# Kernel tuning notes

Hardware: AMD Instinct MI355X
Metric: run time of the kernel (lower is better)

## Reference

```python
import jax, jax.numpy as jnp
import numpy as np

N_QUBITS = 4
N_LAYERS = 3
N_OUTPUTS = 4
BATCH = 1048576


def _ry(t):
    # RY(t) = [[cos(t/2), -sin(t/2)], [sin(t/2), cos(t/2)]]; t may be scalar or (B,)
    c = jnp.cos(t / 2)
    s = jnp.sin(t / 2)
    m = jnp.stack([jnp.stack([c, -s], -1), jnp.stack([s, c], -1)], -2)
    return m.astype(jnp.complex64)


def _rx(t):
    c = jnp.cos(t / 2).astype(jnp.complex64)
    s = jnp.sin(t / 2).astype(jnp.complex64)
    return jnp.stack([jnp.stack([c, -1j * s], -1), jnp.stack([-1j * s, c], -1)], -2)


def _rz(t):
    e = jnp.exp(-1j * t.astype(jnp.complex64) / 2)  # exp(-i t/2)
    z = jnp.zeros_like(e)
    return jnp.stack([jnp.stack([e, z], -1), jnp.stack([z, jnp.conj(e)], -1)], -2)


def _apply_1q(state, U, q):
    # shared 2x2 gate U on wire q; state: (B, 2,2,2,2)
    s = jnp.moveaxis(state, q + 1, -1)
    s = jnp.einsum('ij,...j->...i', U, s)
    return jnp.moveaxis(s, -1, q + 1)


def _apply_1q_batched(state, U, q):
    # per-sample 2x2 gate U: (B,2,2) on wire q
    s = jnp.moveaxis(state, q + 1, -1)  # (B, ..., 2)
    s = jnp.einsum('bij,b...j->b...i', U, s)
    return jnp.moveaxis(s, -1, q + 1)


def _apply_cnot(state, c, t):
    s = jnp.moveaxis(state, (c + 1, t + 1), (-2, -1))  # (..., ctrl, tgt)
    s = jnp.stack([s[..., 0, :], s[..., 1, ::-1]], axis=-2)
    return jnp.moveaxis(s, (-2, -1), (c + 1, t + 1))


def setup_inputs() -> dict:
    key = jax.random.key(0)
    kx, kw = jax.random.split(key)
    x = jax.random.normal(kx, (BATCH, 2), dtype=jnp.float32)
    weights = jax.random.normal(kw, (N_LAYERS, N_QUBITS, 3), dtype=jnp.float32) * 0.1
    return {"x": x, "weights": weights}


def reference(x, weights):
    B = x.shape[0]
    # |0...0> state, batched
    state = jnp.zeros((B,) + (2,) * N_QUBITS, jnp.complex64)
    state = state.at[(slice(None),) + (0,) * N_QUBITS].set(1.0)
    # data encoding: RY(inputs[i % 2]) on wire i (per-sample angles)
    for i in range(N_QUBITS):
        state = _apply_1q_batched(state, _ry(x[:, i % 2]), i)
    # variational layers (shared angles)
    for l in range(N_LAYERS):
        for i in range(N_QUBITS):
            state = _apply_1q(state, _rx(weights[l, i, 0]), i)
            state = _apply_1q(state, _ry(weights[l, i, 1]), i)
            state = _apply_1q(state, _rz(weights[l, i, 2]), i)
        for i in range(N_QUBITS):
            state = _apply_cnot(state, i, (i + 1) % N_QUBITS)
    probs = state.real ** 2 + state.imag ** 2  # (B,2,2,2,2)
    outs = []
    for q in range(N_OUTPUTS):
        p = jnp.moveaxis(probs, q + 1, 1).reshape(B, 2, -1).sum(-1)
        outs.append(p[:, 0] - p[:, 1])  # <Z_q>
    return jnp.stack(outs, -1)  # (B, N_OUTPUTS)
```

## Files before the change

### kernel.cpp

```cpp
#include <hip/hip_runtime.h>
#include <hip/hip_bf16.h>


__device__ __forceinline__ float2 mul2(float2 a, float2 b) {
    return make_float2(a.x * b.x, a.y * b.y);
}
__device__ __forceinline__ float2 fma2(float s, float2 a, float2 b) {
    return make_float2(fmaf(s, a.x, b.x), fmaf(s, a.y, b.y));
}
__device__ __forceinline__ float2 fma22(float2 s, float2 a, float2 b) {
    return make_float2(fmaf(s.x, a.x, b.x), fmaf(s.y, a.y, b.y));
}

__global__ __launch_bounds__(256) void qnn_fused(const float2* __restrict__ x,
                                                 const float* __restrict__ w,
                                                 float4* __restrict__ out,
                                                 int B) {
    __shared__ float Ur[16][16];
    __shared__ float Ui[16][16];
    __shared__ __align__(16) float Csh[100];
    const int t = threadIdx.x;

    if (t < 100) Csh[t] = 0.0f;

    if (t < 16) {
        float ar[16], ai[16];
#pragma unroll
        for (int i = 0; i < 16; i++) { ar[i] = (i == t) ? 1.0f : 0.0f; ai[i] = 0.0f; }

#pragma unroll
        for (int l = 0; l < 3; l++) {
#pragma unroll
            for (int wq = 0; wq < 4; wq++) {
                const int st = 1 << (3 - wq);
                float th, s, c;
                th = w[(l * 4 + wq) * 3 + 0] * 0.5f;
                __sincosf(th, &s, &c);
#pragma unroll
                for (int lo = 0; lo < 16; lo++) if (!(lo & st)) {
                    const int hi = lo | st;
                    const float arl = ar[lo], ail = ai[lo], arh = ar[hi], aih = ai[hi];
                    ar[lo] = c * arl + s * aih;
                    ai[lo] = c * ail - s * arh;
                    ar[hi] = c * arh + s * ail;
                    ai[hi] = c * aih - s * arl;
                }
                th = w[(l * 4 + wq) * 3 + 1] * 0.5f;
                __sincosf(th, &s, &c);
#pragma unroll
                for (int lo = 0; lo < 16; lo++) if (!(lo & st)) {
                    const int hi = lo | st;
                    const float arl = ar[lo], ail = ai[lo], arh = ar[hi], aih = ai[hi];
                    ar[lo] = c * arl - s * arh;
                    ai[lo] = c * ail - s * aih;
                    ar[hi] = s * arl + c * arh;
                    ai[hi] = s * ail + c * aih;
                }
                th = w[(l * 4 + wq) * 3 + 2] * 0.5f;
                __sincosf(th, &s, &c);
#pragma unroll
                for (int lo = 0; lo < 16; lo++) if (!(lo & st)) {
                    const int hi = lo | st;
                    const float arl = ar[lo], ail = ai[lo], arh = ar[hi], aih = ai[hi];
                    ar[lo] = c * arl + s * ail;
                    ai[lo] = c * ail - s * arl;
                    ar[hi] = c * arh - s * aih;
                    ai[hi] = c * aih + s * arh;
                }
            }
#pragma unroll
            for (int ci = 0; ci < 4; ci++) {
                const int cst = 1 << (3 - ci);
                const int tst = 1 << (3 - ((ci + 1) & 3));
#pragma unroll
                for (int k = 0; k < 16; k++) if ((k & cst) && !(k & tst)) {
                    const int k2 = k | tst;
                    const float tr = ar[k], ti = ai[k];
                    ar[k] = ar[k2]; ai[k] = ai[k2];
                    ar[k2] = tr;    ai[k2] = ti;
                }
            }
        }
#pragma unroll
        for (int i = 0; i < 16; i++) { Ur[i][t] = ar[i]; Ui[i][t] = ai[i]; }
    }
    __syncthreads();

    {
        const int i = t >> 4;
        const int j = t & 15;
        float m0 = 0.f, m1 = 0.f, m2 = 0.f, m3 = 0.f;
#pragma unroll
        for (int k = 0; k < 16; k++) {
            const float r = Ur[k][i] * Ur[k][j] + Ui[k][i] * Ui[k][j];
            m0 += ((k >> 3) & 1) ? -r : r;
            m1 += ((k >> 2) & 1) ? -r : r;
            m2 += ((k >> 1) & 1) ? -r : r;
            m3 += ((k >> 0) & 1) ? -r : r;
        }
        const int mm = ((i >> 3) & 1) + ((i >> 1) & 1) + ((j >> 3) & 1) + ((j >> 1) & 1);
        const int nn = ((i >> 2) & 1) + (i & 1) + ((j >> 2) & 1) + (j & 1);
        atomicAdd(&Csh[0 * 25 + mm * 5 + nn], m0);
        atomicAdd(&Csh[1 * 25 + mm * 5 + nn], m1);
        atomicAdd(&Csh[2 * 25 + mm * 5 + nn], m2);
        atomicAdd(&Csh[3 * 25 + mm * 5 + nn], m3);
    }
    __syncthreads();

    float cf[100];
#pragma unroll
    for (int i = 0; i < 25; i++) {
        const float4 v = ((const float4*)Csh)[i];
        cf[4 * i + 0] = v.x;
        cf[4 * i + 1] = v.y;
        cf[4 * i + 2] = v.z;
        cf[4 * i + 3] = v.w;
    }

    const int bs = blockIdx.x * 1024;

    if (bs + 1024 <= B) {
#pragma unroll
        for (int k = 0; k < 2; k++) {
            const int sA = bs + k * 512 + t;
            const int sB = sA + 256;
            const float2 xA = x[sA];
            const float2 xB = x[sB];
            float2 s0, c0, s1, c1;
            __sincosf(xA.x * 0.5f, &s0.x, &c0.x);
            __sincosf(xB.x * 0.5f, &s0.y, &c0.y);
            __sincosf(xA.y * 0.5f, &s1.x, &c1.x);
            __sincosf(xB.y * 0.5f, &s1.y, &c1.y);

            const float2 cc0 = mul2(c0, c0), ss0 = mul2(s0, s0), cs0 = mul2(c0, s0);
            const float2 cc1 = mul2(c1, c1), ss1 = mul2(s1, s1), cs1 = mul2(c1, s1);
            float2 p0[5] = { mul2(cc0, cc0), mul2(cc0, cs0), mul2(cs0, cs0),
                             mul2(cs0, ss0), mul2(ss0, ss0) };
            float2 p1[5] = { mul2(cc1, cc1), mul2(cc1, cs1), mul2(cs1, cs1),
                             mul2(cs1, ss1), mul2(ss1, ss1) };
            float2 o[4];
#pragma unroll
            for (int q = 0; q < 4; q++) {
                float2 acc = make_float2(0.0f, 0.0f);
#pragma unroll
                for (int m = 0; m < 5; m++) {
                    float2 inner = make_float2(0.0f, 0.0f);
#pragma unroll
                    for (int n = 0; n < 5; n++)
                        inner = fma2(cf[q * 25 + m * 5 + n], p1[n], inner);
                    acc = fma22(p0[m], inner, acc);
                }
                o[q] = acc;
            }
            out[sA] = make_float4(o[0].x, o[1].x, o[2].x, o[3].x);
            out[sB] = make_float4(o[0].y, o[1].y, o[2].y, o[3].y);
        }
    } else {
#pragma unroll
        for (int k = 0; k < 4; k++) {
            const int s = bs + k * 256 + t;
            if (s < B) {
                const float2 xv = x[s];
                float st0, ct0, st1, ct1;
                __sincosf(xv.x * 0.5f, &st0, &ct0);
                __sincosf(xv.y * 0.5f, &st1, &ct1);
                const float cc0 = ct0 * ct0, ss0 = st0 * st0, cs0 = ct0 * st0;
                const float cc1 = ct1 * ct1, ss1 = st1 * st1, cs1 = ct1 * st1;
                float q0[5] = { cc0 * cc0, cc0 * cs0, cs0 * cs0, cs0 * ss0, ss0 * ss0 };
                float q1[5] = { cc1 * cc1, cc1 * cs1, cs1 * cs1, cs1 * ss1, ss1 * ss1 };
                float o[4];
#pragma unroll
                for (int q = 0; q < 4; q++) {
                    float acc = 0.0f;
#pragma unroll
                    for (int m = 0; m < 5; m++) {
                        float inner = 0.0f;
#pragma unroll
                        for (int n = 0; n < 5; n++)
                            inner = fmaf(cf[q * 25 + m * 5 + n], q1[n], inner);
                        acc = fmaf(q0[m], inner, acc);
                    }
                    o[q] = acc;
                }
                out[s] = make_float4(o[0], o[1], o[2], o[3]);
            }
        }
    }
}

extern "C" void kernel_launch(void* const* d_in, const int* in_sizes, int n_in,
                              void* d_out, int out_size, void* d_ws, size_t ws_size,
                              hipStream_t stream) {
    const float* x = (const float*)d_in[0];
    const float* w = (const float*)d_in[1];
    const int B = in_sizes[0] / 2;

    int grid = (B + 1023) / 1024;
    if (grid < 1) grid = 1;
    qnn_fused<<<grid, 256, 0, stream>>>((const float2*)x, w, (float4*)d_out, B);
}
```

Before: 84.13 us.

## Use 1024-thread blocks, float4 input loads, and shared-memory coefficient reads

Blocks grow from 256 to 1024 threads, each covering 4096 samples, so the per-block 16x16 unitary build and coefficient reduction are spread over four times as many samples. Each thread now loads two adjacent samples with one float4 read instead of two float2 reads. The coefficient table is stored interleaved by output (float4 per (m,n) pair) and read from shared memory inside the loop rather than copied into 100 registers. The evaluation is reordered to multiply p0[m]*p1[n] once and accumulate all four outputs, which cuts register pressure but adds LDS reads and reduces block-level parallelism.

```diff
diff --git a/kernel.cpp b/kernel.cpp
--- a/kernel.cpp
+++ b/kernel.cpp
@@ -8,14 +8,11 @@
 __device__ __forceinline__ float2 fma2(float s, float2 a, float2 b) {
     return make_float2(fmaf(s, a.x, b.x), fmaf(s, a.y, b.y));
 }
-__device__ __forceinline__ float2 fma22(float2 s, float2 a, float2 b) {
-    return make_float2(fmaf(s.x, a.x, b.x), fmaf(s.y, a.y, b.y));
-}
 
-__global__ __launch_bounds__(256) void qnn_fused(const float2* __restrict__ x,
-                                                 const float* __restrict__ w,
-                                                 float4* __restrict__ out,
-                                                 int B) {
+__global__ __launch_bounds__(1024) void qnn_fused(const float4* __restrict__ x4,
+                                                  const float* __restrict__ w,
+                                                  float4* __restrict__ out,
+                                                  int B) {
     __shared__ float Ur[16][16];
     __shared__ float Ui[16][16];
     __shared__ __align__(16) float Csh[100];
@@ -86,7 +83,7 @@
     }
     __syncthreads();
 
-    {
+    if (t < 256) {
         const int i = t >> 4;
         const int j = t & 15;
         float m0 = 0.f, m1 = 0.f, m2 = 0.f, m3 = 0.f;
@@ -100,89 +97,78 @@
         }
         const int mm = ((i >> 3) & 1) + ((i >> 1) & 1) + ((j >> 3) & 1) + ((j >> 1) & 1);
         const int nn = ((i >> 2) & 1) + (i & 1) + ((j >> 2) & 1) + (j & 1);
-        atomicAdd(&Csh[0 * 25 + mm * 5 + nn], m0);
-        atomicAdd(&Csh[1 * 25 + mm * 5 + nn], m1);
-        atomicAdd(&Csh[2 * 25 + mm * 5 + nn], m2);
-        atomicAdd(&Csh[3 * 25 + mm * 5 + nn], m3);
+        const int mn4 = (mm * 5 + nn) * 4;
+        atomicAdd(&Csh[mn4 + 0], m0);
+        atomicAdd(&Csh[mn4 + 1], m1);
+        atomicAdd(&Csh[mn4 + 2], m2);
+        atomicAdd(&Csh[mn4 + 3], m3);
     }
     __syncthreads();
 
-    float cf[100];
-#pragma unroll
-    for (int i = 0; i < 25; i++) {
-        const float4 v = ((const float4*)Csh)[i];
-        cf[4 * i + 0] = v.x;
-        cf[4 * i + 1] = v.y;
-        cf[4 * i + 2] = v.z;
-        cf[4 * i + 3] = v.w;
-    }
+    const float4* __restrict__ Csh4 = (const float4*)Csh;
 
-    const int bs = blockIdx.x * 1024;
+    const int bs = blockIdx.x * 4096;
 
-    if (bs + 1024 <= B) {
+    if (bs + 4096 <= B) {
 #pragma unroll
         for (int k = 0; k < 2; k++) {
-            const int sA = bs + k * 512 + t;
-            const int sB = sA + 256;
-            const float2 xA = x[sA];
-            const float2 xB = x[sB];
+            const float4 f4 = x4[(bs >> 1) + k * 1024 + t];
             float2 s0, c0, s1, c1;
-            __sincosf(xA.x * 0.5f, &s0.x, &c0.x);
-            __sincosf(xB.x * 0.5f, &s0.y, &c0.y);
-            __sincosf(xA.y * 0.5f, &s1.x, &c1.x);
-            __sincosf(xB.y * 0.5f, &s1.y, &c1.y);
+            __sincosf(f4.x * 0.5f, &s0.x, &c0.x);
+            __sincosf(f4.z * 0.5f, &s0.y, &c0.y);
+            __sincosf(f4.y * 0.5f, &s1.x, &c1.x);
+            __sincosf(f4.w * 0.5f, &s1.y, &c1.y);
 
             const float2 cc0 = mul2(c0, c0), ss0 = mul2(s0, s0), cs0 = mul2(c0, s0);
             const float2 cc1 = mul2(c1, c1), ss1 = mul2(s1, s1), cs1 = mul2(c1, s1);
-            float2 p0[5] = { mul2(cc0, cc0), mul2(cc0, cs0), mul2(cs0, cs0),
-                             mul2(cs0, ss0), mul2(ss0, ss0) };
-            float2 p1[5] = { mul2(cc1, cc1), mul2(cc1, cs1), mul2(cs1, cs1),
-                             mul2(cs1, ss1), mul2(ss1, ss1) };
-            float2 o[4];
+            const float2 p0[5] = { mul2(cc0, cc0), mul2(cc0, cs0), mul2(cs0, cs0),
+                                   mul2(cs0, ss0), mul2(ss0, ss0) };
+            const float2 p1[5] = { mul2(cc1, cc1), mul2(cc1, cs1), mul2(cs1, cs1),
+                                   mul2(cs1, ss1), mul2(ss1, ss1) };
+
+            float2 a0 = make_float2(0.f, 0.f), a1 = a0, a2 = a0, a3 = a0;
 #pragma unroll
-            for (int q = 0; q < 4; q++) {
-                float2 acc = make_float2(0.0f, 0.0f);
+            for (int m = 0; m < 5; m++)
 #pragma unroll
-                for (int m = 0; m < 5; m++) {
-                    float2 inner = make_float2(0.0f, 0.0f);
-#pragma unroll
-                    for (int n = 0; n < 5; n++)
-                        inner = fma2(cf[q * 25 + m * 5 + n], p1[n], inner);
-                    acc = fma22(p0[m], inner, acc);
+                for (int n = 0; n < 5; n++) {
+                    const float4 cv = Csh4[m * 5 + n];
+                    const float2 pp = mul2(p0[m], p1[n]);
+                    a0 = fma2(cv.x, pp, a0);
+                    a1 = fma2(cv.y, pp, a1);
+                    a2 = fma2(cv.z, pp, a2);
+                    a3 = fma2(cv.w, pp, a3);
                 }
-                o[q] = acc;
-            }
-            out[sA] = make_float4(o[0].x, o[1].x, o[2].x, o[3].x);
-            out[sB] = make_float4(o[0].y, o[1].y, o[2].y, o[3].y);
+            const int s = bs + 2 * (k * 1024 + t);
+            out[s]     = make_float4(a0.x, a1.x, a2.x, a3.x);
+            out[s + 1] = make_float4(a0.y, a1.y, a2.y, a3.y);
         }
     } else {
+        const float2* __restrict__ x2 = (const float2*)x4;
 #pragma unroll
         for (int k = 0; k < 4; k++) {
-            const int s = bs + k * 256 + t;
+            const int s = bs + k * 1024 + t;
             if (s < B) {
-                const float2 xv = x[s];
+                const float2 xv = x2[s];
                 float st0, ct0, st1, ct1;
                 __sincosf(xv.x * 0.5f, &st0, &ct0);
                 __sincosf(xv.y * 0.5f, &st1, &ct1);
                 const float cc0 = ct0 * ct0, ss0 = st0 * st0, cs0 = ct0 * st0;
                 const float cc1 = ct1 * ct1, ss1 = st1 * st1, cs1 = ct1 * st1;
-                float q0[5] = { cc0 * cc0, cc0 * cs0, cs0 * cs0, cs0 * ss0, ss0 * ss0 };
-                float q1[5] = { cc1 * cc1, cc1 * cs1, cs1 * cs1, cs1 * ss1, ss1 * ss1 };
-                float o[4];
+                const float q0[5] = { cc0 * cc0, cc0 * cs0, cs0 * cs0, cs0 * ss0, ss0 * ss0 };
+                const float q1[5] = { cc1 * cc1, cc1 * cs1, cs1 * cs1, cs1 * ss1, ss1 * ss1 };
+                float o0 = 0.f, o1 = 0.f, o2 = 0.f, o3 = 0.f;
 #pragma unroll
-                for (int q = 0; q < 4; q++) {
-                    float acc = 0.0f;
+                for (int m = 0; m < 5; m++)
 #pragma unroll
-                    for (int m = 0; m < 5; m++) {
-                        float inner = 0.0f;
-#pragma unroll
-                        for (int n = 0; n < 5; n++)
-                            inner = fmaf(cf[q * 25 + m * 5 + n], q1[n], inner);
-                        acc = fmaf(q0[m], inner, acc);
+                    for (int n = 0; n < 5; n++) {
+                        const float4 cv = Csh4[m * 5 + n];
+                        const float pp = q0[m] * q1[n];
+                        o0 = fmaf(cv.x, pp, o0);
+                        o1 = fmaf(cv.y, pp, o1);
+                        o2 = fmaf(cv.z, pp, o2);
+                        o3 = fmaf(cv.w, pp, o3);
                     }
-                    o[q] = acc;
-                }
-                out[s] = make_float4(o[0], o[1], o[2], o[3]);
+                out[s] = make_float4(o0, o1, o2, o3);
             }
         }
     }
@@ -195,7 +181,7 @@
     const float* w = (const float*)d_in[1];
     const int B = in_sizes[0] / 2;
 
-    int grid = (B + 1023) / 1024;
+    int grid = (B + 4095) / 4096;
     if (grid < 1) grid = 1;
-    qnn_fused<<<grid, 256, 0, stream>>>((const float2*)x, w, (float4*)d_out, B);
+    qnn_fused<<<grid, 1024, 0, stream>>>((const float4*)x, w, (float4*)d_out, B);
 }
```

Result: no change. 84.19 us (+0.1%).
